# Kernel tuning notes

Hardware: AMD Instinct MI355X
Metric: run time of the kernel (lower is better)

The kernel has to match this reference:

```python
import jax, jax.numpy as jnp
import numpy as np

B, S, H = 1, 2048, 1024          # batch, seq_len, hidden_dim
E, I = 16, 512                    # num_experts, moe_intermediate_size
TOP_K = 4
NORM_TOPK_PROB = True


def setup_inputs() -> dict:
    key = jax.random.key(0)
    k0, k1, k2, k3, k4 = jax.random.split(key, 5)
    scale = 0.02
    return {
        "hidden_states": jax.random.normal(k0, (B, S, H), jnp.float32),
        "w_gate": jax.random.normal(k1, (H, E), jnp.float32) * scale,
        "w_gate_proj": jax.random.normal(k2, (E, H, I), jnp.float32) * scale,
        "w_up_proj": jax.random.normal(k3, (E, H, I), jnp.float32) * scale,
        "w_down_proj": jax.random.normal(k4, (E, I, H), jnp.float32) * scale,
    }


def reference(hidden_states, w_gate, w_gate_proj, w_up_proj, w_down_proj):
    b, s, h = hidden_states.shape
    x = hidden_states.reshape(-1, h)                      # [T, H]
    T = x.shape[0]

    router_logits = x @ w_gate                            # [T, E]
    routing_weights = jax.nn.softmax(router_logits.astype(jnp.float32), axis=-1)
    top_w, sel = jax.lax.top_k(routing_weights, TOP_K)    # [T, K]
    if NORM_TOPK_PROB:
        top_w = top_w / top_w.sum(axis=-1, keepdims=True)
    top_w = top_w.astype(x.dtype)

    # Per-token combine weight for every expert (0 if not in top-k).
    # Mathematically identical to the sort/gather/index_add dispatch loop.
    combine = jnp.zeros((T, E), x.dtype).at[
        jnp.arange(T)[:, None], sel].set(top_w)           # [T, E]

    def expert_step(acc, inp):
        wg, wu, wd, w = inp                               # [H,I],[H,I],[I,H],[T]
        hidden = jax.nn.silu(x @ wg) * (x @ wu)           # [T, I]
        return acc + (hidden @ wd) * w[:, None], None

    out0 = jnp.zeros_like(x)
    out, _ = jax.lax.scan(
        expert_step, out0,
        (w_gate_proj, w_up_proj, w_down_proj, combine.T))
    return out.reshape(b, s, h), router_logits
```

## Files before the change

### kernel.cpp

```cpp
#include <hip/hip_runtime.h>
#include <math.h>

constexpr int TT = 2048;
constexpr int HH = 1024;
constexpr int EE = 16;
constexpr int II = 512;

typedef unsigned short u16;
typedef short s16x8 __attribute__((ext_vector_type(8)));
typedef float f32x4 __attribute__((ext_vector_type(4)));

__device__ __forceinline__ u16 f2bf(float f) {
  unsigned u = __float_as_uint(f);
  u = (u + 0x7fffu + ((u >> 16) & 1u)) >> 16;
  return (u16)u;
}

__device__ __forceinline__ void gl2lds16(const void* g, void* l) {
  __builtin_amdgcn_global_load_lds(
      (const __attribute__((address_space(1))) unsigned*)g,
      (__attribute__((address_space(3))) unsigned*)l, 16, 0, 0);
}


__global__ void cast_x_kernel(const float* __restrict__ x, u16* __restrict__ xb,
                              const float* __restrict__ wg, float* __restrict__ wgT) {
  int b = blockIdx.x;
  if (b < TT * HH / 1024) {
    int i = b * blockDim.x + threadIdx.x;
    float4 v = reinterpret_cast<const float4*>(x)[i];
    ushort4 o;
    o.x = f2bf(v.x); o.y = f2bf(v.y); o.z = f2bf(v.z); o.w = f2bf(v.w);
    reinterpret_cast<ushort4*>(xb)[i] = o;
  } else {
    int i = (b - TT * HH / 1024) * blockDim.x + threadIdx.x;
    int h = i >> 4, e = i & 15;
    wgT[e * HH + h] = wg[i];
  }
}

__global__ __launch_bounds__(256) void wtrans_kernel(
    const float* __restrict__ wgp, const float* __restrict__ wup,
    const float* __restrict__ wdp, u16* __restrict__ wgt,
    u16* __restrict__ wut, u16* __restrict__ wdt) {
  int z = blockIdx.z;
  int e = z & 15, t = z >> 4;
  const float* src; u16* dst; int K, N;
  if (t == 0)      { src = wgp + (size_t)e * HH * II; dst = wgt + (size_t)e * II * HH; K = HH; N = II; }
  else if (t == 1) { src = wup + (size_t)e * HH * II; dst = wut + (size_t)e * II * HH; K = HH; N = II; }
  else             { src = wdp + (size_t)e * II * HH; dst = wdt + (size_t)e * HH * II; K = II; N = HH; }
  int bx = blockIdx.x, by = blockIdx.y;
  if (bx * 64 >= N || by * 64 >= K) return;
  int K0 = by * 64, N0 = bx * 64;

  __shared__ u16 lds[64 * 64];

  int tid = threadIdx.x;
  int KR  = tid >> 4;
  int nc4 = (tid & 15) * 4;
  float4 r[4];
#pragma unroll
  for (int ii = 0; ii < 4; ++ii)
    r[ii] = *reinterpret_cast<const float4*>(&src[(size_t)(K0 + 4 * KR + ii) * N + N0 + nc4]);
  u16 bv[4][4];
#pragma unroll
  for (int ii = 0; ii < 4; ++ii) {
    bv[ii][0] = f2bf(r[ii].x); bv[ii][1] = f2bf(r[ii].y);
    bv[ii][2] = f2bf(r[ii].z); bv[ii][3] = f2bf(r[ii].w);
  }
#pragma unroll
  for (int j = 0; j < 4; ++j) {
    int n = nc4 + j;
    int a = n * 64 + ((KR ^ (n & 15)) << 2);
    uint2 p;
    p.x = (unsigned)bv[0][j] | ((unsigned)bv[1][j] << 16);
    p.y = (unsigned)bv[2][j] | ((unsigned)bv[3][j] << 16);
    *reinterpret_cast<uint2*>(&lds[a]) = p;
  }
  __syncthreads();
  int n  = tid >> 2;
  int kc = tid & 3;
  int m  = n & 15;
#pragma unroll
  for (int c = 0; c < 2; ++c) {
    int g = 4 * c + kc;
    int a0 = n * 64 + (((2 * g)     ^ m) << 2);
    int a1 = n * 64 + (((2 * g + 1) ^ m) << 2);
    uint2 q0 = *reinterpret_cast<const uint2*>(&lds[a0]);
    uint2 q1 = *reinterpret_cast<const uint2*>(&lds[a1]);
    uint4 st; st.x = q0.x; st.y = q0.y; st.z = q1.x; st.w = q1.y;
    *reinterpret_cast<uint4*>(&dst[(size_t)(N0 + n) * K + K0 + 8 * g]) = st;
  }
}

__global__ void router_kernel(const float* __restrict__ x, const float* __restrict__ wgT,
                              float* __restrict__ rl, unsigned* __restrict__ selmask,
                              float* __restrict__ wsel) {
  int lane = threadIdx.x & 63, wv = threadIdx.x >> 6;
  int t = blockIdx.x * 4 + wv;
  const float* xr = x + (size_t)t * HH;
  float xv[16];
#pragma unroll
  for (int i = 0; i < 16; ++i) xv[i] = xr[lane + 64 * i];
  float lg[16];
#pragma unroll
  for (int e = 0; e < 16; ++e) {
    const float* wr = wgT + (size_t)e * HH;
    float p = 0.f;
#pragma unroll
    for (int i = 0; i < 16; ++i) p += xv[i] * wr[lane + 64 * i];
#pragma unroll
    for (int s = 32; s > 0; s >>= 1) p += __shfl_xor(p, s, 64);
    lg[e] = p;
  }
  if (lane < 16) rl[(size_t)t * 16 + lane] = lg[lane];
  unsigned mask = 0;
  int sel[4]; float bl[4];
#pragma unroll
  for (int k = 0; k < 4; ++k) {
    float best = -3.4e38f; int bi = 0;
#pragma unroll
    for (int e = 0; e < 16; ++e) {
      bool ok = !((mask >> e) & 1u) && (lg[e] > best);
      best = ok ? lg[e] : best;
      bi = ok ? e : bi;
    }
    mask |= 1u << bi;
    sel[k] = bi; bl[k] = best;
  }
  float mx = bl[0];
  float wk[4]; float s = 0.f;
#pragma unroll
  for (int k = 0; k < 4; ++k) { wk[k] = expf(bl[k] - mx); s += wk[k]; }
  float inv = 1.f / s;
  if (lane == 0) {
    selmask[t] = (unsigned)sel[0] | ((unsigned)sel[1] << 4) |
                 ((unsigned)sel[2] << 8) | ((unsigned)sel[3] << 12);
    float4 w4 = make_float4(wk[0] * inv, wk[1] * inv, wk[2] * inv, wk[3] * inv);
    reinterpret_cast<float4*>(wsel)[t] = w4;
  }
}

__global__ void build_lists_kernel(const unsigned* __restrict__ selmask,
                                   const float* __restrict__ wsel,
                                   int* __restrict__ counts, int* __restrict__ offsets,
                                   int* __restrict__ tlist, float* __restrict__ wlist) {
  __shared__ int scnt[16];
  int lane = threadIdx.x & 63, e = threadIdx.x >> 6;
  int base = 0;
  for (int t0 = 0; t0 < TT; t0 += 64) {
    int t = t0 + lane;
    unsigned m = selmask[t];
    int k = -1;
#pragma unroll
    for (int j = 0; j < 4; ++j)
      if (((m >> (4 * j)) & 15u) == (unsigned)e) k = j;
    unsigned long long bal = __ballot(k >= 0);
    int pos = base + (int)__popcll(bal & ((1ull << lane) - 1ull));
    if (k >= 0) {
      tlist[e * TT + pos] = t;
      wlist[e * TT + pos] = wsel[t * 4 + k];
    }
    base += (int)__popcll(bal);
  }
  if (lane == 0) scnt[e] = base;
  __syncthreads();
  if (threadIdx.x == 0) {
    int s = 0;
    for (int i = 0; i < 16; ++i) { counts[i] = scnt[i]; offsets[i] = s; s += scnt[i]; }
    offsets[16] = s;
  }
}

__global__ __launch_bounds__(256, 2) void gateup_kernel(
    const u16* __restrict__ xb, const u16* __restrict__ wgt, const u16* __restrict__ wut,
    const int* __restrict__ counts, const int* __restrict__ offsets,
    const int* __restrict__ tlist, const float* __restrict__ wlist,
    u16* __restrict__ hidden) {
  int e = blockIdx.z, mt = blockIdx.y, nt = blockIdx.x;
  int cnt = counts[e];
  if (mt * 128 >= cnt) return;
  __shared__ u16 As[128 * 64];
  __shared__ u16 Bg[64 * 64];
  __shared__ u16 Bu[64 * 64];
  int tid = threadIdx.x, lane = tid & 63, wv = tid >> 6;
  int wm = wv >> 1, wn = wv & 1;
  int srow = lane >> 3;
  int scol = (((lane & 7) ^ srow)) * 8;
  const u16* wgE = wgt + (size_t)e * II * HH;
  const u16* wuE = wut + (size_t)e * II * HH;
  const u16* gp[8];
#pragma unroll
  for (int c = 0; c < 8; ++c) {
    int chunk = c * 4 + wv;
    const u16* p;
    if (chunk < 16) {
      int mi = mt * 128 + chunk * 8 + srow; if (mi >= cnt) mi = cnt - 1;
      int tok = tlist[e * TT + mi];
      p = xb + (size_t)tok * HH + scol;
    } else if (chunk < 24) {
      int n = nt * 64 + (chunk - 16) * 8 + srow;
      p = wgE + (size_t)n * HH + scol;
    } else {
      int n = nt * 64 + (chunk - 24) * 8 + srow;
      p = wuE + (size_t)n * HH + scol;
    }
    gp[c] = p;
  }
  f32x4 accG[4][2] = {}; f32x4 accU[4][2] = {};
  int quad = lane >> 4, colc = lane & 15;
  for (int k0 = 0; k0 < HH; k0 += 64) {
#pragma unroll
    for (int c = 0; c < 8; ++c) {
      int chunk = c * 4 + wv;
      u16* dst = (chunk < 16) ? &As[chunk * 512]
               : (chunk < 24) ? &Bg[(chunk - 16) * 512]
                              : &Bu[(chunk - 24) * 512];
      gl2lds16(gp[c] + k0, dst);
    }
    __syncthreads();
#pragma unroll
    for (int kk = 0; kk < 64; kk += 32) {
      int gl = (kk >> 3) + quad;
      s16x8 a[4], bg[2], bu[2];
#pragma unroll
      for (int f = 0; f < 4; ++f) {
        int m = wm * 64 + f * 16 + colc;
        a[f] = *reinterpret_cast<const s16x8*>(&As[m * 64 + ((gl ^ (m & 7)) << 3)]);
      }
#pragma unroll
      for (int f = 0; f < 2; ++f) {
        int n = wn * 32 + f * 16 + colc;
        bg[f] = *reinterpret_cast<const s16x8*>(&Bg[n * 64 + ((gl ^ (n & 7)) << 3)]);
        bu[f] = *reinterpret_cast<const s16x8*>(&Bu[n * 64 + ((gl ^ (n & 7)) << 3)]);
      }
#pragma unroll
      for (int fm = 0; fm < 4; ++fm)
#pragma unroll
        for (int fn = 0; fn < 2; ++fn) {
          accG[fm][fn] = __builtin_amdgcn_mfma_f32_16x16x32_bf16(a[fm], bg[fn], accG[fm][fn], 0, 0, 0);
          accU[fm][fn] = __builtin_amdgcn_mfma_f32_16x16x32_bf16(a[fm], bu[fn], accU[fm][fn], 0, 0, 0);
        }
    }
    __syncthreads();
  }
  int hb = offsets[e];
#pragma unroll
  for (int fm = 0; fm < 4; ++fm) {
#pragma unroll
    for (int r = 0; r < 4; ++r) {
      int mi = mt * 128 + wm * 64 + fm * 16 + quad * 4 + r;
      if (mi < cnt) {
        float wr = wlist[e * TT + mi];
        u16* hrow = hidden + (size_t)(hb + mi) * II + nt * 64 + wn * 32;
#pragma unroll
        for (int fn = 0; fn < 2; ++fn) {
          float g = accG[fm][fn][r], u = accU[fm][fn][r];
          float hval = wr * u * g / (1.f + expf(-g));
          hrow[fn * 16 + colc] = f2bf(hval);
        }
      }
    }
  }
}

__global__ __launch_bounds__(256, 2) void down_kernel(
    const u16* __restrict__ hidden, const u16* __restrict__ wdt,
    const int* __restrict__ counts, const int* __restrict__ offsets,
    const int* __restrict__ tlist, float* __restrict__ out) {
  int e = blockIdx.z, mt = blockIdx.y, nt = blockIdx.x;
  int cnt = counts[e];
  if (mt * 128 >= cnt) return;
  int hb = offsets[e];
  __shared__ u16 As[128 * 64];
  __shared__ u16 Bs[128 * 64];
  int tid = threadIdx.x, lane = tid & 63, wv = tid >> 6;
  int wm = wv >> 1, wn = wv & 1;
  int srow = lane >> 3;
  int scol = (((lane & 7) ^ srow)) * 8;
  const u16* wdE = wdt + (size_t)e * HH * II;
  const u16* gA[4]; const u16* gB[4];
#pragma unroll
  for (int c = 0; c < 4; ++c) {
    int chunk = c * 4 + wv;
    int row = hb + mt * 128 + chunk * 8 + srow;
    if (row > 8191) row = 8191;
    gA[c] = hidden + (size_t)row * II + scol;
    int n = nt * 128 + chunk * 8 + srow;
    gB[c] = wdE + (size_t)n * II + scol;
  }
  f32x4 acc[4][4] = {};
  int quad = lane >> 4, colc = lane & 15;
  for (int k0 = 0; k0 < II; k0 += 64) {
#pragma unroll
    for (int c = 0; c < 4; ++c) {
      int chunk = c * 4 + wv;
      gl2lds16(gA[c] + k0, &As[chunk * 512]);
      gl2lds16(gB[c] + k0, &Bs[chunk * 512]);
    }
    __syncthreads();
#pragma unroll
    for (int kk = 0; kk < 64; kk += 32) {
      int gl = (kk >> 3) + quad;
      s16x8 a[4], b[4];
#pragma unroll
      for (int f = 0; f < 4; ++f) {
        int m = wm * 64 + f * 16 + colc;
        int n = wn * 64 + f * 16 + colc;
        a[f] = *reinterpret_cast<const s16x8*>(&As[m * 64 + ((gl ^ (m & 7)) << 3)]);
        b[f] = *reinterpret_cast<const s16x8*>(&Bs[n * 64 + ((gl ^ (n & 7)) << 3)]);
      }
#pragma unroll
      for (int fm = 0; fm < 4; ++fm)
#pragma unroll
        for (int fn = 0; fn < 4; ++fn)
          acc[fm][fn] = __builtin_amdgcn_mfma_f32_16x16x32_bf16(a[fm], b[fn], acc[fm][fn], 0, 0, 0);
    }
    __syncthreads();
  }
#pragma unroll
  for (int fm = 0; fm < 4; ++fm) {
#pragma unroll
    for (int r = 0; r < 4; ++r) {
      int mi = mt * 128 + wm * 64 + fm * 16 + quad * 4 + r;
      if (mi < cnt) {
        int tok = tlist[e * TT + mi];
        float* orow = out + (size_t)tok * HH + nt * 128 + wn * 64;
#pragma unroll
        for (int fn = 0; fn < 4; ++fn)
          atomicAdd(&orow[fn * 16 + colc], acc[fm][fn][r]);
      }
    }
  }
}

extern "C" void kernel_launch(void* const* d_in, const int* in_sizes, int n_in,
                              void* d_out, int out_size, void* d_ws, size_t ws_size,
                              hipStream_t stream) {
  const float* x   = (const float*)d_in[0];
  const float* wg  = (const float*)d_in[1];
  const float* wgp = (const float*)d_in[2];
  const float* wup = (const float*)d_in[3];
  const float* wdp = (const float*)d_in[4];
  float* out = (float*)d_out;
  float* rl  = out + (size_t)TT * HH;

  char* w = (char*)d_ws;
  int*      counts  = (int*)(w + 0);
  int*      offsets = (int*)(w + 64);
  unsigned* selmask = (unsigned*)(w + 1024);
  float*    wsel    = (float*)(w + 1024 + 8192);
  int*      tlist   = (int*)(w + 49152);
  float*    wlist   = (float*)(w + 49152 + 131072);
  float*    wgT     = (float*)(w + 49152 + 262144);
  u16*      xb      = (u16*)(w + 49152 + 262144 + 65536);
  u16*      wgt     = xb  + (size_t)TT * HH;
  u16*      wut     = wgt + (size_t)EE * II * HH;
  u16*      wdt     = wut + (size_t)EE * II * HH;
  u16*      hidden  = wdt + (size_t)EE * HH * II;

  hipMemsetAsync(out, 0, (size_t)TT * HH * sizeof(float), stream);

  hipLaunchKernelGGL(cast_x_kernel, dim3(TT * HH / 1024 + 64), dim3(256), 0, stream,
                     x, xb, wg, wgT);
  hipLaunchKernelGGL(wtrans_kernel, dim3(16, 16, 48), dim3(256), 0, stream,
                     wgp, wup, wdp, wgt, wut, wdt);
  hipLaunchKernelGGL(router_kernel, dim3(TT / 4), dim3(256), 0, stream,
                     x, wgT, rl, selmask, wsel);
  hipLaunchKernelGGL(build_lists_kernel, dim3(1), dim3(1024), 0, stream,
                     selmask, wsel, counts, offsets, tlist, wlist);
  hipLaunchKernelGGL(gateup_kernel, dim3(8, 16, 16), dim3(256), 0, stream,
                     xb, wgt, wut, counts, offsets, tlist, wlist, hidden);
  hipLaunchKernelGGL(down_kernel, dim3(8, 16, 16), dim3(256), 0, stream,
                     hidden, wdt, counts, offsets, tlist, out);
}
```

Baseline: 255.8 us.

## Replace atomic scatter with bf16 staging plus combine kernel; rewrite weight transpose

The down projection now writes bf16 per-(token,expert) rows into a scratch buffer, which reuses the gate-weight workspace. A new combine kernel gathers each token's four rows using a rowof map built in build_lists, replacing the memset and fp32 atomicAdds into the output. The weight transpose kernel drops its LDS staging: each thread reads 8 rows of float4 and writes packed 16-byte bf16 columns directly, on a flat 1D grid. This adds an extra kernel plus bf16 rounding of the per-expert outputs before summation, and build_lists now makes two passes over the selections.

New measurement: 244.2 us. -4.6%, faster.

```diff
diff --git a/kernel.cpp b/kernel.cpp
--- a/kernel.cpp
+++ b/kernel.cpp
@@ -15,13 +15,15 @@
   u = (u + 0x7fffu + ((u >> 16) & 1u)) >> 16;
   return (u16)u;
 }
+__device__ __forceinline__ float bf2f(u16 b) {
+  return __uint_as_float(((unsigned)b) << 16);
+}
 
 __device__ __forceinline__ void gl2lds16(const void* g, void* l) {
   __builtin_amdgcn_global_load_lds(
       (const __attribute__((address_space(1))) unsigned*)g,
       (__attribute__((address_space(3))) unsigned*)l, 16, 0, 0);
 }
-
 
 __global__ void cast_x_kernel(const float* __restrict__ x, u16* __restrict__ xb,
                               const float* __restrict__ wg, float* __restrict__ wgT) {
@@ -43,53 +45,35 @@
     const float* __restrict__ wgp, const float* __restrict__ wup,
     const float* __restrict__ wdp, u16* __restrict__ wgt,
     u16* __restrict__ wut, u16* __restrict__ wdt) {
-  int z = blockIdx.z;
+  int bid = blockIdx.x;
+  int z = bid >> 6, lb = bid & 63;
   int e = z & 15, t = z >> 4;
   const float* src; u16* dst; int K, N;
   if (t == 0)      { src = wgp + (size_t)e * HH * II; dst = wgt + (size_t)e * II * HH; K = HH; N = II; }
   else if (t == 1) { src = wup + (size_t)e * HH * II; dst = wut + (size_t)e * II * HH; K = HH; N = II; }
   else             { src = wdp + (size_t)e * II * HH; dst = wdt + (size_t)e * HH * II; K = II; N = HH; }
-  int bx = blockIdx.x, by = blockIdx.y;
-  if (bx * 64 >= N || by * 64 >= K) return;
-  int K0 = by * 64, N0 = bx * 64;
-
-  __shared__ u16 lds[64 * 64];
-
+  int nTiles = N >> 8;
+  int n0 = (lb % nTiles) * 256;
+  int k0 = (lb / nTiles) * 32;
   int tid = threadIdx.x;
-  int KR  = tid >> 4;
-  int nc4 = (tid & 15) * 4;
-  float4 r[4];
-#pragma unroll
-  for (int ii = 0; ii < 4; ++ii)
-    r[ii] = *reinterpret_cast<const float4*>(&src[(size_t)(K0 + 4 * KR + ii) * N + N0 + nc4]);
-  u16 bv[4][4];
-#pragma unroll
-  for (int ii = 0; ii < 4; ++ii) {
-    bv[ii][0] = f2bf(r[ii].x); bv[ii][1] = f2bf(r[ii].y);
-    bv[ii][2] = f2bf(r[ii].z); bv[ii][3] = f2bf(r[ii].w);
-  }
-#pragma unroll
-  for (int j = 0; j < 4; ++j) {
-    int n = nc4 + j;
-    int a = n * 64 + ((KR ^ (n & 15)) << 2);
-    uint2 p;
-    p.x = (unsigned)bv[0][j] | ((unsigned)bv[1][j] << 16);
-    p.y = (unsigned)bv[2][j] | ((unsigned)bv[3][j] << 16);
-    *reinterpret_cast<uint2*>(&lds[a]) = p;
-  }
-  __syncthreads();
-  int n  = tid >> 2;
-  int kc = tid & 3;
-  int m  = n & 15;
-#pragma unroll
-  for (int c = 0; c < 2; ++c) {
-    int g = 4 * c + kc;
-    int a0 = n * 64 + (((2 * g)     ^ m) << 2);
-    int a1 = n * 64 + (((2 * g + 1) ^ m) << 2);
-    uint2 q0 = *reinterpret_cast<const uint2*>(&lds[a0]);
-    uint2 q1 = *reinterpret_cast<const uint2*>(&lds[a1]);
-    uint4 st; st.x = q0.x; st.y = q0.y; st.z = q1.x; st.w = q1.y;
-    *reinterpret_cast<uint4*>(&dst[(size_t)(N0 + n) * K + K0 + 8 * g]) = st;
+  int ng = (tid & 63) * 4;
+  int kk = k0 + (tid >> 6) * 8;
+  float4 r[8];
+#pragma unroll
+  for (int j = 0; j < 8; ++j)
+    r[j] = *reinterpret_cast<const float4*>(&src[(size_t)(kk + j) * N + n0 + ng]);
+#pragma unroll
+  for (int nn = 0; nn < 4; ++nn) {
+    float v[8];
+#pragma unroll
+    for (int j = 0; j < 8; ++j)
+      v[j] = (nn == 0) ? r[j].x : (nn == 1) ? r[j].y : (nn == 2) ? r[j].z : r[j].w;
+    uint4 st;
+    st.x = (unsigned)f2bf(v[0]) | ((unsigned)f2bf(v[1]) << 16);
+    st.y = (unsigned)f2bf(v[2]) | ((unsigned)f2bf(v[3]) << 16);
+    st.z = (unsigned)f2bf(v[4]) | ((unsigned)f2bf(v[5]) << 16);
+    st.w = (unsigned)f2bf(v[6]) | ((unsigned)f2bf(v[7]) << 16);
+    *reinterpret_cast<uint4*>(&dst[(size_t)(n0 + ng + nn) * K + kk]) = st;
   }
 }
 
@@ -144,10 +128,30 @@
 __global__ void build_lists_kernel(const unsigned* __restrict__ selmask,
                                    const float* __restrict__ wsel,
                                    int* __restrict__ counts, int* __restrict__ offsets,
-                                   int* __restrict__ tlist, float* __restrict__ wlist) {
+                                   int* __restrict__ tlist, float* __restrict__ wlist,
+                                   int* __restrict__ rowof) {
   __shared__ int scnt[16];
+  __shared__ int soff[16];
   int lane = threadIdx.x & 63, e = threadIdx.x >> 6;
   int base = 0;
+  for (int t0 = 0; t0 < TT; t0 += 64) {
+    unsigned m = selmask[t0 + lane];
+    bool hit = false;
+#pragma unroll
+    for (int j = 0; j < 4; ++j)
+      hit |= (((m >> (4 * j)) & 15u) == (unsigned)e);
+    base += (int)__popcll(__ballot(hit));
+  }
+  if (lane == 0) scnt[e] = base;
+  __syncthreads();
+  if (threadIdx.x == 0) {
+    int s = 0;
+    for (int i = 0; i < 16; ++i) { counts[i] = scnt[i]; offsets[i] = s; soff[i] = s; s += scnt[i]; }
+    offsets[16] = s;
+  }
+  __syncthreads();
+  int hb = soff[e];
+  base = 0;
   for (int t0 = 0; t0 < TT; t0 += 64) {
     int t = t0 + lane;
     unsigned m = selmask[t];
@@ -160,15 +164,9 @@
     if (k >= 0) {
       tlist[e * TT + pos] = t;
       wlist[e * TT + pos] = wsel[t * 4 + k];
+      rowof[t * 4 + k] = hb + pos;
     }
     base += (int)__popcll(bal);
-  }
-  if (lane == 0) scnt[e] = base;
-  __syncthreads();
-  if (threadIdx.x == 0) {
-    int s = 0;
-    for (int i = 0; i < 16; ++i) { counts[i] = scnt[i]; offsets[i] = s; s += scnt[i]; }
-    offsets[16] = s;
   }
 }
 
@@ -267,7 +265,7 @@
 __global__ __launch_bounds__(256, 2) void down_kernel(
     const u16* __restrict__ hidden, const u16* __restrict__ wdt,
     const int* __restrict__ counts, const int* __restrict__ offsets,
-    const int* __restrict__ tlist, float* __restrict__ out) {
+    u16* __restrict__ dtmp) {
   int e = blockIdx.z, mt = blockIdx.y, nt = blockIdx.x;
   int cnt = counts[e];
   if (mt * 128 >= cnt) return;
@@ -324,14 +322,28 @@
     for (int r = 0; r < 4; ++r) {
       int mi = mt * 128 + wm * 64 + fm * 16 + quad * 4 + r;
       if (mi < cnt) {
-        int tok = tlist[e * TT + mi];
-        float* orow = out + (size_t)tok * HH + nt * 128 + wn * 64;
+        u16* drow = dtmp + (size_t)(hb + mi) * HH + nt * 128 + wn * 64;
 #pragma unroll
         for (int fn = 0; fn < 4; ++fn)
-          atomicAdd(&orow[fn * 16 + colc], acc[fm][fn][r]);
-      }
-    }
-  }
+          drow[fn * 16 + colc] = f2bf(acc[fm][fn][r]);
+      }
+    }
+  }
+}
+
+__global__ void combine_kernel(const u16* __restrict__ dtmp, const int* __restrict__ rowof,
+                               float* __restrict__ out) {
+  int t = blockIdx.x, tid = threadIdx.x;
+  int4 rw = reinterpret_cast<const int4*>(rowof)[t];
+  int h = tid * 4;
+  float s0 = 0.f, s1 = 0.f, s2 = 0.f, s3 = 0.f;
+  int rows[4] = {rw.x, rw.y, rw.z, rw.w};
+#pragma unroll
+  for (int k = 0; k < 4; ++k) {
+    ushort4 v = *reinterpret_cast<const ushort4*>(&dtmp[(size_t)rows[k] * HH + h]);
+    s0 += bf2f(v.x); s1 += bf2f(v.y); s2 += bf2f(v.z); s3 += bf2f(v.w);
+  }
+  *reinterpret_cast<float4*>(&out[(size_t)t * HH + h]) = make_float4(s0, s1, s2, s3);
 }
 
 extern "C" void kernel_launch(void* const* d_in, const int* in_sizes, int n_in,
@@ -349,28 +361,30 @@
   int*      counts  = (int*)(w + 0);
   int*      offsets = (int*)(w + 64);
   unsigned* selmask = (unsigned*)(w + 1024);
-  float*    wsel    = (float*)(w + 1024 + 8192);
-  int*      tlist   = (int*)(w + 49152);
-  float*    wlist   = (float*)(w + 49152 + 131072);
-  float*    wgT     = (float*)(w + 49152 + 262144);
-  u16*      xb      = (u16*)(w + 49152 + 262144 + 65536);
+  float*    wsel    = (float*)(w + 16384);
+  int*      rowof   = (int*)(w + 49152);
+  int*      tlist   = (int*)(w + 81920);
+  float*    wlist   = (float*)(w + 210944);
+  float*    wgT     = (float*)(w + 339968);
+  u16*      xb      = (u16*)(w + 405504);
   u16*      wgt     = xb  + (size_t)TT * HH;
   u16*      wut     = wgt + (size_t)EE * II * HH;
   u16*      wdt     = wut + (size_t)EE * II * HH;
   u16*      hidden  = wdt + (size_t)EE * HH * II;
-
-  hipMemsetAsync(out, 0, (size_t)TT * HH * sizeof(float), stream);
+  u16*      dtmp    = wgt;
 
   hipLaunchKernelGGL(cast_x_kernel, dim3(TT * HH / 1024 + 64), dim3(256), 0, stream,
                      x, xb, wg, wgT);
-  hipLaunchKernelGGL(wtrans_kernel, dim3(16, 16, 48), dim3(256), 0, stream,
+  hipLaunchKernelGGL(wtrans_kernel, dim3(3072), dim3(256), 0, stream,
                      wgp, wup, wdp, wgt, wut, wdt);
   hipLaunchKernelGGL(router_kernel, dim3(TT / 4), dim3(256), 0, stream,
                      x, wgT, rl, selmask, wsel);
   hipLaunchKernelGGL(build_lists_kernel, dim3(1), dim3(1024), 0, stream,
-                     selmask, wsel, counts, offsets, tlist, wlist);
+                     selmask, wsel, counts, offsets, tlist, wlist, rowof);
   hipLaunchKernelGGL(gateup_kernel, dim3(8, 16, 16), dim3(256), 0, stream,
                      xb, wgt, wut, counts, offsets, tlist, wlist, hidden);
   hipLaunchKernelGGL(down_kernel, dim3(8, 16, 16), dim3(256), 0, stream,
-                     hidden, wdt, counts, offsets, tlist, out);
-}
+                     hidden, wdt, counts, offsets, dtmp);
+  hipLaunchKernelGGL(combine_kernel, dim3(TT), dim3(256), 0, stream,
+                     dtmp, rowof, out);
+}
```
